# Performance work log

Hardware: AMD Instinct MI355X
Metric: run time of the kernel (lower is better)

The kernel has to match this reference:

```python
import jax, jax.numpy as jnp
import numpy as np
import math

B, N, D = 4, 2048, 512
H, DH = 8, 128
INNER = H * DH


def setup_inputs() -> dict:
    key = jax.random.key(0)
    k1, k2, k3, k4 = jax.random.split(key, 4)
    x = jax.random.normal(k1, (B, N, D), dtype=jnp.float32)
    Wg = jax.random.normal(k2, (D, INNER), dtype=jnp.float32) * (1.0 / math.sqrt(D))
    Wout = jax.random.normal(k3, (INNER, D), dtype=jnp.float32) * (1.0 / math.sqrt(INNER))
    sigma = jax.random.uniform(k4, (1, H, 1, 1), dtype=jnp.float32, minval=0.5, maxval=2.5)
    return {"x": x, "Wg": Wg, "Wout": Wout, "sigma": sigma}


def reference(x, Wg, Wout, sigma):
    b, n, d = x.shape
    h, dh = H, DH
    # value projection: [b,n,d] @ [d, h*dh] -> [b,h,n,dh]
    v = (x @ Wg).reshape(b, n, h, dh).transpose(0, 2, 1, 3)
    # fixed Gaussian positional mask, shared across batch: build once per head
    pos = jnp.arange(1, n + 1, dtype=jnp.float32)
    diffs = jnp.abs(pos[:, None] - pos[None, :])  # [n, n]
    sig = sigma.reshape(h, 1, 1)  # [h,1,1]
    inv_norm = 1.0 / (jnp.sqrt(2.0 * jnp.float32(math.pi)) * sig)
    gauss = inv_norm * jnp.exp(-(diffs[None] ** 2) / (2.0 * sig ** 2))  # [h,n,n]
    corr = gauss / gauss.sum(-1, keepdims=True)  # row-normalized [h,n,n]
    # attention: broadcast mask over batch
    attn = jnp.einsum('hnm,bhmd->bhnd', corr, v)
    out = attn.transpose(0, 2, 1, 3).reshape(b, n, h * dh)
    return out @ Wout  # dropout p=0.0 -> identity
```

## Files before the change

### kernel.cpp

```cpp
#include <hip/hip_runtime.h>
#include <hip/hip_bf16.h>
#include <math.h>

#define B_ 4
#define N_ 2048
#define D_ 512
#define H_ 8
#define DH_ 128
#define INNER_ 1024
#define W_ 32
#define M_ (B_ * N_)

typedef __attribute__((ext_vector_type(8))) short short8;
typedef __attribute__((ext_vector_type(4))) float floatx4;

typedef const __attribute__((address_space(1))) char* gcp;
typedef __attribute__((address_space(3))) char* lcp;

__device__ __forceinline__ unsigned f_to_bf16bits(float f) {
    union { float f; unsigned u; } c; c.f = f;
    return (c.u + 0x7fffu + ((c.u >> 16) & 1u)) >> 16;
}
__device__ __forceinline__ float bf16s_to_f(unsigned short s) {
    union { unsigned u; float f; } c; c.u = ((unsigned)s) << 16; return c.f;
}

#define VST2 200
#define AROWS 192
#define BOFF 24576

__global__ __launch_bounds__(512, 4) void g1_blur(
    const __hip_bfloat16* __restrict__ x_bf,
    const __hip_bfloat16* __restrict__ Wg_t,
    const float* __restrict__ sigma,
    const float* __restrict__ winv_g,
    __hip_bfloat16* __restrict__ attn)
{
    __shared__ char smem[51456];

    const int tid  = threadIdx.x;
    const int lane = tid & 63;
    const int w    = tid >> 6;
    const int wm   = w >> 1;
    const int wn   = w & 1;
    const int quad = lane >> 4;
    const int cl   = lane & 15;

    const int L    = blockIdx.x + 64 * blockIdx.y;
    const int xcd  = L & 7;
    const int idx  = L >> 3;
    const int bm   = xcd * 8 + (idx & 7);
    const int h    = idx >> 3;
    const int n0   = bm * 128;
    const int nb0  = n0 & (N_ - 1);

    floatx4 acc[3][4];
    #pragma unroll
    for (int i = 0; i < 3; ++i)
        #pragma unroll
        for (int j = 0; j < 4; ++j) acc[i][j] = (floatx4){0.f, 0.f, 0.f, 0.f};

    const char* Ab = (const char*)x_bf;
    const char* Bb = (const char*)(Wg_t + (size_t)(h * DH_) * D_);

    for (int k0 = 0; k0 < D_; k0 += 64) {
        #pragma unroll
        for (int it = 0; it < 3; ++it) {
            int o = it * 8192 + tid * 16;
            int r = o >> 7;
            int c = ((o >> 4) & 7) ^ (r & 7);
            int gr = n0 - W_ + r;
            gr = gr < 0 ? 0 : (gr > M_ - 1 ? M_ - 1 : gr);
            __builtin_amdgcn_global_load_lds(
                (gcp)(Ab + (size_t)gr * 1024 + k0 * 2 + c * 16), (lcp)(smem + o), 16, 0, 0);
        }
        #pragma unroll
        for (int it = 0; it < 2; ++it) {
            int o = it * 8192 + tid * 16;
            int r = o >> 7;
            int c = ((o >> 4) & 7) ^ (r & 7);
            __builtin_amdgcn_global_load_lds(
                (gcp)(Bb + (size_t)r * 1024 + k0 * 2 + c * 16), (lcp)(smem + BOFF + o), 16, 0, 0);
        }
        __syncthreads();

        const short* As = (const short*)smem;
        const short* Bs = (const short*)(smem + BOFF);
        #pragma unroll
        for (int kk = 0; kk < 2; ++kk) {
            short8 af[3], bf[4];
            int ch = kk * 4 + quad;
            #pragma unroll
            for (int t = 0; t < 3; ++t) {
                int ra = wm * 48 + t * 16 + cl;
                af[t] = *(const short8*)(As + ra * 64 + ((ch ^ (ra & 7)) * 8));
            }
            #pragma unroll
            for (int t = 0; t < 4; ++t) {
                int rb = wn * 64 + t * 16 + cl;
                bf[t] = *(const short8*)(Bs + rb * 64 + ((ch ^ (rb & 7)) * 8));
            }
            #pragma unroll
            for (int i = 0; i < 3; ++i)
                #pragma unroll
                for (int j = 0; j < 4; ++j)
                    acc[i][j] = __builtin_amdgcn_mfma_f32_16x16x32_bf16(
                        af[i], bf[j], acc[i][j], 0, 0, 0);
        }
        __syncthreads();
    }

    float wv[2][4];
    #pragma unroll
    for (int mi = 0; mi < 2; ++mi)
        #pragma unroll
        for (int r = 0; r < 4; ++r)
            wv[mi][r] = winv_g[h * N_ + nb0 + wm * 32 + mi * 16 + quad * 4 + r];

    unsigned short* vsT   = (unsigned short*)smem;
    unsigned short* wtabS = (unsigned short*)(smem + 51200);

    #pragma unroll
    for (int i = 0; i < 3; ++i) {
        #pragma unroll
        for (int j = 0; j < 4; ++j) {
            int ch   = wn * 64 + j * 16 + cl;
            int row0 = wm * 48 + i * 16 + quad * 4;
            unsigned p01 = 0u, p23 = 0u;
            #pragma unroll
            for (int rr = 0; rr < 4; ++rr) {
                int vb = nb0 - W_ + row0 + rr;
                unsigned bits = (vb >= 0 && vb < N_) ? f_to_bf16bits(acc[i][j][rr]) : 0u;
                if (rr < 2) p01 |= bits << (rr * 16);
                else        p23 |= bits << ((rr - 2) * 16);
            }
            unsigned* dst = (unsigned*)(vsT + ch * VST2 + row0);
            dst[0] = p01; dst[1] = p23;
        }
    }
    if (tid <= 2 * W_) {
        float sig = sigma[h];
        float d = (float)(tid - W_);
        wtabS[tid] = (unsigned short)f_to_bf16bits(__expf(-d * d / (2.0f * sig * sig)));
    }
    __syncthreads();

    short afr[2][3][8];
    #pragma unroll
    for (int mi = 0; mi < 2; ++mi) {
        int row = wm * 32 + mi * 16 + cl;
        #pragma unroll
        for (int t = 0; t < 3; ++t) {
            int lb = (wm + t) * 32 + quad * 8 - row;
            #pragma unroll
            for (int j = 0; j < 8; ++j) {
                int l = lb + j;
                afr[mi][t][j] = (l >= 0 && l <= 2 * W_) ? (short)wtabS[l] : (short)0;
            }
        }
    }

    floatx4 oacc[2][4];
    #pragma unroll
    for (int mi = 0; mi < 2; ++mi)
        #pragma unroll
        for (int ni = 0; ni < 4; ++ni) oacc[mi][ni] = (floatx4){0.f, 0.f, 0.f, 0.f};

    #pragma unroll
    for (int t = 0; t < 3; ++t) {
        int k32 = wm + t;
        short8 bfr[4];
        #pragma unroll
        for (int ni = 0; ni < 4; ++ni) {
            int ch = wn * 64 + ni * 16 + cl;
            bfr[ni] = *(const short8*)((const short*)vsT + ch * VST2 + k32 * 32 + quad * 8);
        }
        #pragma unroll
        for (int mi = 0; mi < 2; ++mi)
            #pragma unroll
            for (int ni = 0; ni < 4; ++ni)
                oacc[mi][ni] = __builtin_amdgcn_mfma_f32_16x16x32_bf16(
                    *(short8*)afr[mi][t], bfr[ni], oacc[mi][ni], 0, 0, 0);
    }

    #pragma unroll
    for (int mi = 0; mi < 2; ++mi) {
        #pragma unroll
        for (int ni = 0; ni < 4; ++ni) {
            int ch = wn * 64 + ni * 16 + cl;
            #pragma unroll
            for (int r = 0; r < 4; ++r) {
                int orow = wm * 32 + mi * 16 + quad * 4 + r;
                attn[(size_t)(n0 + orow) * INNER_ + h * DH_ + ch] =
                    __float2bfloat16(oacc[mi][ni][r] * wv[mi][r]);
            }
        }
    }
}

__global__ __launch_bounds__(256, 3) void gemm2_dbuf(
    const __hip_bfloat16* __restrict__ A,
    const __hip_bfloat16* __restrict__ Bt,
    float* __restrict__ C)
{
    __shared__ char smem[49152];

    const int bid  = blockIdx.x;
    const int xcd  = bid & 7;
    const int idx  = bid >> 3;
    const int bm   = xcd * 16 + (idx & 15);
    const int bn   = idx >> 4;

    const int tid  = threadIdx.x;
    const int lane = tid & 63;
    const int w    = tid >> 6;
    const int wm   = w >> 1;
    const int wn   = w & 1;
    const int kh   = lane >> 4;
    const int ml   = lane & 15;

    floatx4 acc[2][4];
    #pragma unroll
    for (int i = 0; i < 2; ++i)
        #pragma unroll
        for (int j = 0; j < 4; ++j) acc[i][j] = (floatx4){0.f, 0.f, 0.f, 0.f};

    const char* Ab = (const char*)(A + (size_t)(bm * 64) * INNER_);
    const char* Bb = (const char*)(Bt + (size_t)(bn * 128) * INNER_);

    auto issue = [&](int buf, int k0) {
        #pragma unroll
        for (int it = 0; it < 2; ++it) {
            int o = it * 4096 + tid * 16;
            int r = o >> 7;
            int c = ((o >> 4) & 7) ^ (r & 7);
            __builtin_amdgcn_global_load_lds(
                (gcp)(Ab + (size_t)r * 2048 + k0 * 2 + c * 16),
                (lcp)(smem + buf * 24576 + o), 16, 0, 0);
        }
        #pragma unroll
        for (int it = 0; it < 4; ++it) {
            int o = it * 4096 + tid * 16;
            int r = o >> 7;
            int c = ((o >> 4) & 7) ^ (r & 7);
            __builtin_amdgcn_global_load_lds(
                (gcp)(Bb + (size_t)r * 2048 + k0 * 2 + c * 16),
                (lcp)(smem + buf * 24576 + 8192 + o), 16, 0, 0);
        }
    };
    auto consume = [&](int buf) {
        const short* As = (const short*)(smem + buf * 24576);
        const short* Bs = (const short*)(smem + buf * 24576 + 8192);
        short8 af[2][2], bf[4][2];
        #pragma unroll
        for (int t = 0; t < 2; ++t) {
            int ra = wm * 32 + t * 16 + ml;
            #pragma unroll
            for (int kk = 0; kk < 2; ++kk) {
                int ch = kk * 4 + kh;
                af[t][kk] = *(const short8*)(As + ra * 64 + ((ch ^ (ra & 7)) * 8));
            }
        }
        #pragma unroll
        for (int ni = 0; ni < 4; ++ni) {
            int rb = wn * 64 + ni * 16 + ml;
            #pragma unroll
            for (int kk = 0; kk < 2; ++kk) {
                int ch = kk * 4 + kh;
                bf[ni][kk] = *(const short8*)(Bs + rb * 64 + ((ch ^ (rb & 7)) * 8));
            }
        }
        #pragma unroll
        for (int kk = 0; kk < 2; ++kk)
            #pragma unroll
            for (int i = 0; i < 2; ++i)
                #pragma unroll
                for (int j = 0; j < 4; ++j)
                    acc[i][j] = __builtin_amdgcn_mfma_f32_16x16x32_bf16(
                        af[i][kk], bf[j][kk], acc[i][j], 0, 0, 0);
    };

    const int nk = INNER_ >> 6;
    issue(0, 0);
    for (int kt = 0; kt < nk; kt += 2) {
        __syncthreads();
        if (kt + 1 < nk) issue(1, (kt + 1) << 6);
        consume(0);
        __syncthreads();
        if (kt + 2 < nk) issue(0, (kt + 2) << 6);
        consume(1);
    }
    __syncthreads();

    float* Cs = (float*)smem;
    const int rq = lane >> 4;
    const int cl = lane & 15;
    #pragma unroll
    for (int i = 0; i < 2; ++i)
        #pragma unroll
        for (int j = 0; j < 4; ++j)
            #pragma unroll
            for (int r = 0; r < 4; ++r)
                Cs[(wm * 32 + i * 16 + rq * 4 + r) * 128 + wn * 64 + j * 16 + cl] = acc[i][j][r];
    __syncthreads();

    #pragma unroll
    for (int p = 0; p < 8; ++p) {
        int idx2 = p * 256 + tid;
        int rr = idx2 >> 5;
        int cc = (idx2 & 31) * 4;
        float4 vv = *(const float4*)(Cs + rr * 128 + cc);
        *(float4*)(C + (size_t)(bm * 64 + rr) * D_ + bn * 128 + cc) = vv;
    }
}

__device__ __forceinline__ void transpose32(
    const float* __restrict__ src, __hip_bfloat16* __restrict__ dst,
    int R, int Cn, int rt, int ct, int tid)
{
    __shared__ float t[32][33];
    int c0 = ct * 32, r0 = rt * 32;
    int lx = tid & 31, ly = tid >> 5;
    #pragma unroll
    for (int i = 0; i < 32; i += 8)
        t[ly + i][lx] = src[(size_t)(r0 + ly + i) * Cn + c0 + lx];
    __syncthreads();
    #pragma unroll
    for (int i = 0; i < 32; i += 8)
        dst[(size_t)(c0 + ly + i) * R + r0 + lx] = __float2bfloat16(t[lx][ly + i]);
}

__global__ __launch_bounds__(256) void prep(
    const float* __restrict__ x, const float* __restrict__ Wg,
    const float* __restrict__ Wout, const float* __restrict__ sigma,
    __hip_bfloat16* __restrict__ x_bf, __hip_bfloat16* __restrict__ Wg_t,
    __hip_bfloat16* __restrict__ Wout_t, float* __restrict__ winv_g)
{
    const int bid = blockIdx.x;
    const int tid = threadIdx.x;
    if (bid < 2048) {
        int i = bid * 256 + tid;
        const float4* s = (const float4*)x + (size_t)i * 2;
        float4 a = s[0], b = s[1];
        __hip_bfloat16 o[8] = {
            __float2bfloat16(a.x), __float2bfloat16(a.y), __float2bfloat16(a.z), __float2bfloat16(a.w),
            __float2bfloat16(b.x), __float2bfloat16(b.y), __float2bfloat16(b.z), __float2bfloat16(b.w)};
        *(short8*)(x_bf + (size_t)i * 8) = *(short8*)o;
    } else if (bid < 2560) {
        int id2 = bid - 2048;
        transpose32(Wg, Wg_t, D_, INNER_, id2 >> 5, id2 & 31, tid);
    } else if (bid < 3072) {
        int id2 = bid - 2560;
        transpose32(Wout, Wout_t, INNER_, D_, id2 >> 4, id2 & 15, tid);
    } else {
        int idx = (bid - 3072) * 256 + tid;
        int hh = idx >> 11;
        int n  = idx & (N_ - 1);
        float sig = sigma[hh];
        float ws = 0.f;
        for (int l = 0; l <= 2 * W_; ++l) {
            int vb = n + l - W_;
            if (vb >= 0 && vb < N_) {
                float d = (float)(l - W_);
                ws += bf16s_to_f((unsigned short)f_to_bf16bits(
                    __expf(-d * d / (2.0f * sig * sig))));
            }
        }
        winv_g[idx] = 1.0f / ws;
    }
}

extern "C" void kernel_launch(void* const* d_in, const int* in_sizes, int n_in,
                              void* d_out, int out_size, void* d_ws, size_t ws_size,
                              hipStream_t stream) {
    const float* x     = (const float*)d_in[0];
    const float* Wg    = (const float*)d_in[1];
    const float* Wout  = (const float*)d_in[2];
    const float* sigma = (const float*)d_in[3];
    float* out = (float*)d_out;

    char* ws = (char*)d_ws;
    __hip_bfloat16* x_bf   = (__hip_bfloat16*)ws;
    __hip_bfloat16* Wg_t   = (__hip_bfloat16*)(ws + (((size_t)8)  << 20));
    __hip_bfloat16* Wout_t = (__hip_bfloat16*)(ws + (((size_t)9)  << 20));
    __hip_bfloat16* attn   = (__hip_bfloat16*)(ws + (((size_t)10) << 20));
    float*          winv_g = (float*)(ws + (((size_t)26) << 20));

    prep<<<dim3(3136), dim3(256), 0, stream>>>(x, Wg, Wout, sigma,
                                               x_bf, Wg_t, Wout_t, winv_g);

    g1_blur<<<dim3(64, H_), dim3(512), 0, stream>>>(x_bf, Wg_t, sigma, winv_g, attn);

    gemm2_dbuf<<<dim3(512), dim3(256), 0, stream>>>(attn, Wout_t, out);
}
```

Measured before the change: 112.3 us.

## Enlarge output GEMM tile to 128x128 with single-buffered LDS and direct stores

Rewrites the final projection GEMM to use 128x128 block tiles (256 blocks instead of 512), so each wave computes a 64x64 sub-tile with more MFMA reuse per LDS fragment load. Double buffering is dropped in favour of a single 32KB buffer with load-sync-compute-sync, and the LDS-staged coalesced epilogue is replaced by direct scalar fp32 stores from the accumulators. This cuts redundant A/B loads and LDS use, and targets four blocks per CU. In exchange it loses load/compute overlap, halves the block count on a 256-CU part, and writes the output with less coalesced stores.

After: 117.6 us. 1.05x slower.

```diff
diff --git a/kernel.cpp b/kernel.cpp
--- a/kernel.cpp
+++ b/kernel.cpp
@@ -26,7 +26,6 @@
 }
 
 #define VST2 200
-#define AROWS 192
 #define BOFF 24576
 
 __global__ __launch_bounds__(512, 4) void g1_blur(
@@ -198,119 +197,83 @@
     }
 }
 
-__global__ __launch_bounds__(256, 3) void gemm2_dbuf(
+__global__ __launch_bounds__(256, 4) void gemm2_m97(
     const __hip_bfloat16* __restrict__ A,
     const __hip_bfloat16* __restrict__ Bt,
     float* __restrict__ C)
 {
-    __shared__ char smem[49152];
-
-    const int bid  = blockIdx.x;
-    const int xcd  = bid & 7;
-    const int idx  = bid >> 3;
-    const int bm   = xcd * 16 + (idx & 15);
-    const int bn   = idx >> 4;
+    __shared__ char smem[32768];
+
+    const int L    = blockIdx.x;
+    const int xcd  = L & 7;
+    const int idx  = L >> 3;
+    const int bm   = xcd * 8 + (idx & 7);
+    const int bn   = idx >> 3;
 
     const int tid  = threadIdx.x;
     const int lane = tid & 63;
     const int w    = tid >> 6;
     const int wm   = w >> 1;
     const int wn   = w & 1;
-    const int kh   = lane >> 4;
-    const int ml   = lane & 15;
-
-    floatx4 acc[2][4];
-    #pragma unroll
-    for (int i = 0; i < 2; ++i)
+    const int quad = lane >> 4;
+    const int cl   = lane & 15;
+
+    floatx4 acc[4][4];
+    #pragma unroll
+    for (int i = 0; i < 4; ++i)
         #pragma unroll
         for (int j = 0; j < 4; ++j) acc[i][j] = (floatx4){0.f, 0.f, 0.f, 0.f};
 
-    const char* Ab = (const char*)(A + (size_t)(bm * 64) * INNER_);
+    const char* Ab = (const char*)(A + (size_t)(bm * 128) * INNER_);
     const char* Bb = (const char*)(Bt + (size_t)(bn * 128) * INNER_);
 
-    auto issue = [&](int buf, int k0) {
-        #pragma unroll
-        for (int it = 0; it < 2; ++it) {
-            int o = it * 4096 + tid * 16;
-            int r = o >> 7;
-            int c = ((o >> 4) & 7) ^ (r & 7);
-            __builtin_amdgcn_global_load_lds(
-                (gcp)(Ab + (size_t)r * 2048 + k0 * 2 + c * 16),
-                (lcp)(smem + buf * 24576 + o), 16, 0, 0);
-        }
+    for (int k0 = 0; k0 < INNER_; k0 += 64) {
         #pragma unroll
         for (int it = 0; it < 4; ++it) {
             int o = it * 4096 + tid * 16;
             int r = o >> 7;
             int c = ((o >> 4) & 7) ^ (r & 7);
             __builtin_amdgcn_global_load_lds(
-                (gcp)(Bb + (size_t)r * 2048 + k0 * 2 + c * 16),
-                (lcp)(smem + buf * 24576 + 8192 + o), 16, 0, 0);
-        }
-    };
-    auto consume = [&](int buf) {
-        const short* As = (const short*)(smem + buf * 24576);
-        const short* Bs = (const short*)(smem + buf * 24576 + 8192);
-        short8 af[2][2], bf[4][2];
-        #pragma unroll
-        for (int t = 0; t < 2; ++t) {
-            int ra = wm * 32 + t * 16 + ml;
-            #pragma unroll
-            for (int kk = 0; kk < 2; ++kk) {
-                int ch = kk * 4 + kh;
-                af[t][kk] = *(const short8*)(As + ra * 64 + ((ch ^ (ra & 7)) * 8));
-            }
-        }
-        #pragma unroll
-        for (int ni = 0; ni < 4; ++ni) {
-            int rb = wn * 64 + ni * 16 + ml;
-            #pragma unroll
-            for (int kk = 0; kk < 2; ++kk) {
-                int ch = kk * 4 + kh;
-                bf[ni][kk] = *(const short8*)(Bs + rb * 64 + ((ch ^ (rb & 7)) * 8));
-            }
-        }
-        #pragma unroll
-        for (int kk = 0; kk < 2; ++kk)
-            #pragma unroll
-            for (int i = 0; i < 2; ++i)
+                (gcp)(Ab + (size_t)r * 2048 + k0 * 2 + c * 16), (lcp)(smem + o), 16, 0, 0);
+            __builtin_amdgcn_global_load_lds(
+                (gcp)(Bb + (size_t)r * 2048 + k0 * 2 + c * 16), (lcp)(smem + 16384 + o), 16, 0, 0);
+        }
+        __syncthreads();
+
+        const short* As = (const short*)smem;
+        const short* Bs = (const short*)(smem + 16384);
+        #pragma unroll
+        for (int kk = 0; kk < 2; ++kk) {
+            short8 af[4], bf[4];
+            int ch = kk * 4 + quad;
+            #pragma unroll
+            for (int t = 0; t < 4; ++t) {
+                int ra = wm * 64 + t * 16 + cl;
+                int rb = wn * 64 + t * 16 + cl;
+                af[t] = *(const short8*)(As + ra * 64 + ((ch ^ (ra & 7)) * 8));
+                bf[t] = *(const short8*)(Bs + rb * 64 + ((ch ^ (rb & 7)) * 8));
+            }
+            #pragma unroll
+            for (int i = 0; i < 4; ++i)
                 #pragma unroll
                 for (int j = 0; j < 4; ++j)
                     acc[i][j] = __builtin_amdgcn_mfma_f32_16x16x32_bf16(
-                        af[i][kk], bf[j][kk], acc[i][j], 0, 0, 0);
-    };
-
-    const int nk = INNER_ >> 6;
-    issue(0, 0);
-    for (int kt = 0; kt < nk; kt += 2) {
+                        af[i], bf[j], acc[i][j], 0, 0, 0);
+        }
         __syncthreads();
-        if (kt + 1 < nk) issue(1, (kt + 1) << 6);
-        consume(0);
-        __syncthreads();
-        if (kt + 2 < nk) issue(0, (kt + 2) << 6);
-        consume(1);
-    }
-    __syncthreads();
-
-    float* Cs = (float*)smem;
-    const int rq = lane >> 4;
-    const int cl = lane & 15;
-    #pragma unroll
-    for (int i = 0; i < 2; ++i)
-        #pragma unroll
-        for (int j = 0; j < 4; ++j)
-            #pragma unroll
-            for (int r = 0; r < 4; ++r)
-                Cs[(wm * 32 + i * 16 + rq * 4 + r) * 128 + wn * 64 + j * 16 + cl] = acc[i][j][r];
-    __syncthreads();
-
-    #pragma unroll
-    for (int p = 0; p < 8; ++p) {
-        int idx2 = p * 256 + tid;
-        int rr = idx2 >> 5;
-        int cc = (idx2 & 31) * 4;
-        float4 vv = *(const float4*)(Cs + rr * 128 + cc);
-        *(float4*)(C + (size_t)(bm * 64 + rr) * D_ + bn * 128 + cc) = vv;
+    }
+
+    #pragma unroll
+    for (int i = 0; i < 4; ++i) {
+        #pragma unroll
+        for (int j = 0; j < 4; ++j) {
+            int col = bn * 128 + wn * 64 + j * 16 + cl;
+            #pragma unroll
+            for (int r = 0; r < 4; ++r) {
+                int row = bm * 128 + wm * 64 + i * 16 + quad * 4 + r;
+                C[(size_t)row * D_ + col] = acc[i][j][r];
+            }
+        }
     }
 }
 
@@ -391,5 +354,5 @@
 
     g1_blur<<<dim3(64, H_), dim3(512), 0, stream>>>(x_bf, Wg_t, sigma, winv_g, attn);
 
-    gemm2_dbuf<<<dim3(512), dim3(256), 0, stream>>>(attn, Wout_t, out);
-}
+    gemm2_m97<<<dim3(256), dim3(256), 0, stream>>>(attn, Wout_t, out);
+}
```
